# Performance work log

Measured on AMD Instinct MI355X. Metric: run time of the kernel, lower is better.

## Reference

```python
import jax, jax.numpy as jnp
import numpy as np

N, E, F_IN, HID, HEADS, B, CLASSES = 50000, 800000, 128, 64, 4, 512, 2


def setup_inputs() -> dict:
    key = jax.random.key(0)
    ks = jax.random.split(key, 20)
    s = 0.05
    inp = {
        "x": jax.random.normal(ks[0], (N, F_IN), jnp.float32),
        "edge_index": jax.random.randint(ks[1], (2, E), 0, N, jnp.int32),
        "batch": jnp.sort(jax.random.randint(ks[2], (N,), 0, B, jnp.int32)),
        # GCN layers (3): layer0 F_IN->HID, layers 1,2 HID->HID
        "gcn_w0": jax.random.normal(ks[3], (F_IN, HID), jnp.float32) * s,
        "gcn_b0": jnp.zeros((HID,), jnp.float32),
        "gcn_w1": jax.random.normal(ks[4], (HID, HID), jnp.float32) * s,
        "gcn_b1": jnp.zeros((HID,), jnp.float32),
        "gcn_w2": jax.random.normal(ks[5], (HID, HID), jnp.float32) * s,
        "gcn_b2": jnp.zeros((HID,), jnp.float32),
        # GAT: W [HID, HEADS*HID], attention vectors [HEADS, HID], bias [HID] (concat=False)
        "gat_w": jax.random.normal(ks[6], (HID, HEADS * HID), jnp.float32) * s,
        "gat_att_src": jax.random.normal(ks[7], (HEADS, HID), jnp.float32) * s,
        "gat_att_dst": jax.random.normal(ks[8], (HEADS, HID), jnp.float32) * s,
        "gat_b": jnp.zeros((HID,), jnp.float32),
        # MLP head
        "lin1_w": jax.random.normal(ks[9], (HID, HID // 2), jnp.float32) * s,
        "lin1_b": jnp.zeros((HID // 2,), jnp.float32),
        "lin2_w": jax.random.normal(ks[10], (HID // 2, CLASSES), jnp.float32) * s,
        "lin2_b": jnp.zeros((CLASSES,), jnp.float32),
    }
    return inp


def _forward(x, edge_index, batch,
             gcn_w0, gcn_b0, gcn_w1, gcn_b1, gcn_w2, gcn_b2,
             gat_w, gat_att_src, gat_att_dst, gat_b,
             lin1_w, lin1_b, lin2_w, lin2_b):
    n = x.shape[0]
    loop = jnp.arange(n, dtype=edge_index.dtype)
    src = jnp.concatenate([edge_index[0], loop])  # [E+N] with self-loops
    dst = jnp.concatenate([edge_index[1], loop])

    # symmetric GCN normalization (self-loops included, deg >= 1)
    deg = jax.ops.segment_sum(jnp.ones_like(dst, dtype=x.dtype), dst, num_segments=n)
    dinv = jax.lax.rsqrt(jnp.maximum(deg, 1.0))
    norm = dinv[src] * dinv[dst]  # [E+N]

    for W, b in ((gcn_w0, gcn_b0), (gcn_w1, gcn_b1), (gcn_w2, gcn_b2)):
        h = x @ W  # [N, HID]
        x = jax.ops.segment_sum(h[src] * norm[:, None], dst, num_segments=n) + b
        x = jax.nn.relu(x)  # dropout is identity in eval mode

    # GAT layer (heads=HEADS, concat=False -> mean over heads)
    H, C = gat_att_src.shape
    h = (x @ gat_w).reshape(n, H, C)  # [N, H, C]
    a_src = jnp.einsum('nhc,hc->nh', h, gat_att_src)
    a_dst = jnp.einsum('nhc,hc->nh', h, gat_att_dst)
    e = jax.nn.leaky_relu(a_src[src] + a_dst[dst], 0.2)  # [E+N, H]
    m = jax.ops.segment_max(e, dst, num_segments=n)      # per-dst softmax max
    p = jnp.exp(e - m[dst])
    denom = jax.ops.segment_sum(p, dst, num_segments=n)
    alpha = p / denom[dst]                                # [E+N, H]
    out = jax.ops.segment_sum(h[src] * alpha[:, :, None], dst, num_segments=n)
    x = jax.nn.relu(out.mean(axis=1) + gat_b)             # [N, HID]

    # global mean pool + global max pool over graphs
    cnt = jax.ops.segment_sum(jnp.ones((n,), x.dtype), batch, num_segments=B)
    mean_p = jax.ops.segment_sum(x, batch, num_segments=B) / jnp.maximum(cnt, 1.0)[:, None]
    max_p = jax.ops.segment_max(x, batch, num_segments=B)
    max_p = jnp.where(cnt[:, None] > 0, max_p, 0.0)
    g = mean_p + max_p  # [B, HID]

    g = jax.nn.relu(g @ lin1_w + lin1_b)
    return g @ lin2_w + lin2_b  # [B, CLASSES]


def reference(x, edge_index, batch,
              gcn_w0, gcn_b0, gcn_w1, gcn_b1, gcn_w2, gcn_b2,
              gat_w, gat_att_src, gat_att_dst, gat_b,
              lin1_w, lin1_b, lin2_w, lin2_b):
    return _forward(x, edge_index, batch,
                    gcn_w0, gcn_b0, gcn_w1, gcn_b1, gcn_w2, gcn_b2,
                    gat_w, gat_att_src, gat_att_dst, gat_b,
                    lin1_w, lin1_b, lin2_w, lin2_b)
```

## Files before the change

kernel.cpp:

```cpp
#include <hip/hip_runtime.h>
#include <math.h>

typedef short bf8 __attribute__((ext_vector_type(8)));
typedef _Float16 h8 __attribute__((ext_vector_type(8)));
typedef float f4 __attribute__((ext_vector_type(4)));
typedef unsigned short ushort_t;

#define BRANGE 128
#define NB_E 256

__device__ __forceinline__ int ilanebcast(int v, int l) {
  return __builtin_amdgcn_readlane(v, l);
}

__device__ __forceinline__ float wave_sum(float v) {
#pragma unroll
  for (int off = 32; off > 0; off >>= 1) v += __shfl_xor(v, off, 64);
  return v;
}

__device__ __forceinline__ ushort_t f2bf(float x) {
  unsigned int u = __float_as_uint(x);
  return (ushort_t)((u + 0x7fffu + ((u >> 16) & 1u)) >> 16);
}
__device__ __forceinline__ float b2f(ushort_t h) {
  return __uint_as_float(((unsigned int)h) << 16);
}

__global__ __launch_bounds__(256) void k_ehist(const int* __restrict__ dst,
                                               int* __restrict__ bhistT, int E, int nbuk) {
  __shared__ int h[512];
  int b = blockIdx.x, tid = threadIdx.x;
  for (int i = tid; i < nbuk; i += 256) h[i] = 0;
  __syncthreads();
  int chunk = (E + gridDim.x - 1) / gridDim.x;
  int e0 = b * chunk, e1 = min(E, e0 + chunk);
  for (int e = e0 + tid; e < e1; e += 256) atomicAdd(&h[dst[e] >> 7], 1);
  __syncthreads();
  for (int i = tid; i < nbuk; i += 256) bhistT[i * NB_E + b] = h[i];
}

__global__ __launch_bounds__(256) void k_btot(const int* __restrict__ bhistT,
                                              int* __restrict__ bcnt, int nb) {
  __shared__ int sm[256];
  int b = blockIdx.x, tid = threadIdx.x;
  sm[tid] = (tid < nb) ? bhistT[b * NB_E + tid] : 0;
  __syncthreads();
  for (int off = 128; off > 0; off >>= 1) {
    if (tid < off) sm[tid] += sm[tid + off];
    __syncthreads();
  }
  if (tid == 0) bcnt[b] = sm[0];
}

__global__ __launch_bounds__(512) void k_bscan(
    const int* __restrict__ bcnt, int* __restrict__ edgebase, int nbuk,
    int* __restrict__ rowstart, int n, int E) {
  __shared__ int smem[512];
  int t = threadIdx.x;
  int v = (t < nbuk) ? bcnt[t] : 0;
  smem[t] = v;
  __syncthreads();
  for (int off = 1; off < 512; off <<= 1) {
    int u = (t >= off) ? smem[t - off] : 0;
    __syncthreads();
    smem[t] += u;
    __syncthreads();
  }
  if (t < nbuk) edgebase[t] = smem[t] - v;
  if (t == 0) rowstart[n] = E + n;
}

__global__ __launch_bounds__(256) void k_bbase(int* __restrict__ bhistT,
                                               const int* __restrict__ edgebase,
                                               int nb) {
  __shared__ int sm[256];
  int b = blockIdx.x, tid = threadIdx.x;
  int v = (tid < nb) ? bhistT[b * NB_E + tid] : 0;
  sm[tid] = v;
  __syncthreads();
  for (int off = 1; off < 256; off <<= 1) {
    int u = (tid >= off) ? sm[tid - off] : 0;
    __syncthreads();
    sm[tid] += u;
    __syncthreads();
  }
  if (tid < nb) bhistT[b * NB_E + tid] = edgebase[b] + sm[tid] - v;
}

__global__ __launch_bounds__(256) void k_ebucket(
    const int* __restrict__ es, const int* __restrict__ ed,
    const int* __restrict__ bhistT, int* __restrict__ bedges, int E, int nbuk) {
  __shared__ int cur[512];
  int b = blockIdx.x, tid = threadIdx.x;
  for (int i = tid; i < nbuk; i += 256) cur[i] = bhistT[i * NB_E + b];
  __syncthreads();
  int chunk = (E + gridDim.x - 1) / gridDim.x;
  int e0 = b * chunk, e1 = min(E, e0 + chunk);
  for (int e = e0 + tid; e < e1; e += 256) {
    int s = es[e], d = ed[e];
    int pos = atomicAdd(&cur[d >> 7], 1);
    bedges[pos] = (s << 7) | (d & 127);
  }
}

__global__ __launch_bounds__(256) void k_ebsort(
    const int* __restrict__ bedges, const int* __restrict__ edgebase,
    const int* __restrict__ bcnt, int* __restrict__ colidx,
    int* __restrict__ rowstart, float* __restrict__ dinv, int n) {
  __shared__ int h[128];
  __shared__ int c[128];
  int b = blockIdx.x, tid = threadIdx.x;
  int nodes0 = b * BRANGE;
  int nnode = min(BRANGE, n - nodes0);
  int ebase = edgebase[b], ecnt = bcnt[b];
  int colbase = ebase + nodes0;
  if (tid < 128) h[tid] = (tid < nnode) ? 1 : 0;
  __syncthreads();
  for (int k = ebase + tid; k < ebase + ecnt; k += 256)
    atomicAdd(&h[bedges[k] & 127], 1);
  __syncthreads();
  int own = (tid < 128) ? h[tid] : 0;
  for (int off = 1; off < 128; off <<= 1) {
    int t = (tid >= off && tid < 128) ? h[tid - off] : 0;
    __syncthreads();
    if (tid < 128) h[tid] += t;
    __syncthreads();
  }
  if (tid < nnode) {
    int excl = h[tid] - own;
    int node = nodes0 + tid;
    rowstart[node] = colbase + excl;
    dinv[node] = 1.0f / sqrtf((float)own);
    colidx[colbase + excl] = node;
    c[tid] = excl + 1;
  }
  __syncthreads();
  for (int k = ebase + tid; k < ebase + ecnt; k += 256) {
    int p = bedges[k];
    int pos = atomicAdd(&c[p & 127], 1);
    colidx[colbase + pos] = p >> 7;
  }
}


__global__ void k_wswz0(const float* __restrict__ W, ushort_t* __restrict__ Bh,
                        ushort_t* __restrict__ Bl) {
  int e = blockIdx.x * 256 + threadIdx.x;
  if (e >= 4 * 4 * 64) return;
  int lane = e & 63, kc = (e >> 6) & 3, ct = e >> 8;
  int k0 = kc * 32 + (lane >> 4) * 8;
  int col = ct * 16 + (lane & 15);
#pragma unroll
  for (int j = 0; j < 8; j++) {
    float w = W[(k0 + j) * 64 + col];
    ushort_t h = f2bf(w);
    Bh[(size_t)e * 8 + j] = h;
    Bl[(size_t)e * 8 + j] = f2bf(w - b2f(h));
  }
}

__global__ void k_wswz1(const float* __restrict__ W, _Float16* __restrict__ Bh,
                        _Float16* __restrict__ Bl) {
  int e = blockIdx.x * 256 + threadIdx.x;
  if (e >= 8 * 64) return;
  int lane = e & 63, kc = (e >> 6) & 1, ct = e >> 7;
  int k0 = kc * 32 + (lane >> 4) * 8;
  int col = ct * 16 + (lane & 15);
#pragma unroll
  for (int j = 0; j < 8; j++) {
    float w = W[(k0 + j) * 64 + col];
    _Float16 h = (_Float16)w;
    Bh[(size_t)e * 8 + j] = h;
    Bl[(size_t)e * 8 + j] = (_Float16)(w - (float)h);
  }
}

__global__ void k_wswzg(const float* __restrict__ W, ushort_t* __restrict__ Bh,
                        ushort_t* __restrict__ Bl) {
  int e = blockIdx.x * 256 + threadIdx.x;
  if (e >= 4 * 8 * 64) return;
  int lane = e & 63, kc = (e >> 6) & 7, ct = e >> 9;
  int k0 = kc * 32 + (lane >> 4) * 8;
  int col = ct * 16 + (lane & 15);
#pragma unroll
  for (int j = 0; j < 8; j++) {
    int k = k0 + j;
    float w = W[(k & 63) * 256 + (k >> 6) * 64 + col];
    ushort_t h = f2bf(w);
    Bh[(size_t)e * 8 + j] = h;
    Bl[(size_t)e * 8 + j] = f2bf(w - b2f(h));
  }
}

__global__ void k_qpre(const float* __restrict__ W, const float* __restrict__ att_s,
                       const float* __restrict__ att_d,
                       float* __restrict__ q_src, float* __restrict__ q_dst) {
  int t = threadIdx.x;
  int h = t >> 6, k = t & 63;
  float ss = 0.0f, sd = 0.0f;
  for (int c = 0; c < 64; c++) {
    float w = W[k * 256 + h * 64 + c];
    ss = fmaf(w, att_s[h * 64 + c], ss);
    sd = fmaf(w, att_d[h * 64 + c], sd);
  }
  q_src[h * 64 + k] = ss;
  q_dst[h * 64 + k] = sd;
}

__global__ void k_qswz(const float* __restrict__ q_src, const float* __restrict__ q_dst,
                       _Float16* __restrict__ Bq) {
  int e = threadIdx.x;
  if (e >= 128) return;
  int lane = e & 63, kc = e >> 6;
  int k0 = kc * 32 + (lane >> 4) * 8;
  int col = lane & 15;
#pragma unroll
  for (int j = 0; j < 8; j++) {
    int k = k0 + j;
    float v = (col < 4) ? q_src[col * 64 + k]
                        : ((col < 8) ? q_dst[(col - 4) * 64 + k] : 0.0f);
    Bq[(size_t)e * 8 + j] = (_Float16)v;
  }
}

__global__ __launch_bounds__(256) void k_gemm0_mfma(
    const float* __restrict__ X, const ushort_t* __restrict__ Bh,
    const ushort_t* __restrict__ Bl, const float* __restrict__ dinv,
    _Float16* __restrict__ H, int n, int ntiles) {
  int tid = threadIdx.x, lane = tid & 63, wave = tid >> 6;
  int m = lane & 15, q = lane >> 4;
  for (int tile = blockIdx.x * 4 + wave; tile < ntiles; tile += gridDim.x * 4) {
    int ra = tile * 16 + m;
    if (ra >= n) ra = n - 1;
    const float* xrow = X + (size_t)ra * 128;
    f4 acc[4];
#pragma unroll
    for (int ct = 0; ct < 4; ct++) acc[ct] = (f4){0.f, 0.f, 0.f, 0.f};
#pragma unroll 2
    for (int kc = 0; kc < 4; kc++) {
      int ko = kc * 32 + q * 8;
      float4 xa = *(const float4*)(xrow + ko);
      float4 xb = *(const float4*)(xrow + ko + 4);
      float f[8] = {xa.x, xa.y, xa.z, xa.w, xb.x, xb.y, xb.z, xb.w};
      union { ushort_t u[8]; bf8 v; } Uh, Ul;
#pragma unroll
      for (int j = 0; j < 8; j++) {
        ushort_t h = f2bf(f[j]);
        Uh.u[j] = h;
        Ul.u[j] = f2bf(f[j] - b2f(h));
      }
#pragma unroll
      for (int ct = 0; ct < 4; ct++) {
        size_t boff = ((size_t)(ct * 4 + kc) * 64 + lane) * 8;
        bf8 bh = *(const bf8*)(Bh + boff);
        bf8 bl = *(const bf8*)(Bl + boff);
        acc[ct] = __builtin_amdgcn_mfma_f32_16x16x32_bf16(Uh.v, bh, acc[ct], 0, 0, 0);
        acc[ct] = __builtin_amdgcn_mfma_f32_16x16x32_bf16(Ul.v, bh, acc[ct], 0, 0, 0);
        acc[ct] = __builtin_amdgcn_mfma_f32_16x16x32_bf16(Uh.v, bl, acc[ct], 0, 0, 0);
      }
    }
#pragma unroll
    for (int r = 0; r < 4; r++) {
      int row = tile * 16 + q * 4 + r;
      if (row < n) {
        float dv = dinv[row];
#pragma unroll
        for (int ct = 0; ct < 4; ct++)
          H[(size_t)row * 64 + ct * 16 + m] = (_Float16)(acc[ct][r] * dv);
      }
    }
  }
}

__device__ __forceinline__ float gather_sum(const _Float16* __restrict__ h_in,
                                            const int* __restrict__ colidx,
                                            int s0, int s1, int lane) {
  float acc = 0.0f, accB = 0.0f;
  for (int base = s0; base < s1; base += 64) {
    int cnt = min(64, s1 - base);
    int myidx = (lane < cnt) ? colidx[base + lane] : 0;
    int k = 0;
    for (; k + 3 < cnt; k += 4) {
      int sa = ilanebcast(myidx, k);
      int sb = ilanebcast(myidx, k + 1);
      int sc = ilanebcast(myidx, k + 2);
      int sd = ilanebcast(myidx, k + 3);
      float va = (float)h_in[((size_t)sa << 6) + lane];
      float vb = (float)h_in[((size_t)sb << 6) + lane];
      float vc = (float)h_in[((size_t)sc << 6) + lane];
      float vd = (float)h_in[((size_t)sd << 6) + lane];
      acc += va; accB += vb; acc += vc; accB += vd;
    }
    for (; k < cnt; k++) {
      int sa = ilanebcast(myidx, k);
      acc += (float)h_in[((size_t)sa << 6) + lane];
    }
  }
  return acc + accB;
}

__global__ __launch_bounds__(1024) void k_agg_gemm_mfma(
    const _Float16* __restrict__ h_in, const float* __restrict__ dinv,
    const int* __restrict__ rowstart, const int* __restrict__ colidx,
    const float* __restrict__ bias, const _Float16* __restrict__ Bh,
    const _Float16* __restrict__ Bl, _Float16* __restrict__ h_out, int n) {
  __shared__ __align__(16) _Float16 xstage[16][72];
  int tid = threadIdx.x, lane = tid & 63, w = tid >> 6;
  int tile = blockIdx.x;
  int node = tile * 16 + w;
  float xv = 0.0f;
  if (node < n) {
    int s0 = rowstart[node], s1 = rowstart[node + 1];
    float a = gather_sum(h_in, colidx, s0, s1, lane);
    xv = fmaxf(fmaf(dinv[node], a, bias[lane]), 0.0f);
  }
  xstage[w][lane] = (_Float16)xv;
  __syncthreads();
  if (w < 4) {
    int m = lane & 15, q = lane >> 4, ct = w;
    h8 af0 = *(const h8*)&xstage[m][q * 8];
    h8 af1 = *(const h8*)&xstage[m][32 + q * 8];
    size_t o0 = ((size_t)(ct * 2 + 0) * 64 + lane) * 8;
    size_t o1 = ((size_t)(ct * 2 + 1) * 64 + lane) * 8;
    h8 bh0 = *(const h8*)(Bh + o0);
    h8 bh1 = *(const h8*)(Bh + o1);
    h8 bl0 = *(const h8*)(Bl + o0);
    h8 bl1 = *(const h8*)(Bl + o1);
    f4 acc = (f4){0.f, 0.f, 0.f, 0.f};
    acc = __builtin_amdgcn_mfma_f32_16x16x32_f16(af0, bh0, acc, 0, 0, 0);
    acc = __builtin_amdgcn_mfma_f32_16x16x32_f16(af1, bh1, acc, 0, 0, 0);
    acc = __builtin_amdgcn_mfma_f32_16x16x32_f16(af0, bl0, acc, 0, 0, 0);
    acc = __builtin_amdgcn_mfma_f32_16x16x32_f16(af1, bl1, acc, 0, 0, 0);
#pragma unroll
    for (int r = 0; r < 4; r++) {
      int n2 = tile * 16 + q * 4 + r;
      if (n2 < n)
        h_out[(size_t)n2 * 64 + ct * 16 + m] = (_Float16)(acc[r] * dinv[n2]);
    }
  }
}

__global__ __launch_bounds__(1024) void k_agg_gatpre_mfma(
    const _Float16* __restrict__ h_in, const float* __restrict__ dinv,
    const int* __restrict__ rowstart, const int* __restrict__ colidx,
    const float* __restrict__ bias, const _Float16* __restrict__ Bq,
    _Float16* __restrict__ x3, float* __restrict__ a_src, float* __restrict__ a_dst,
    int n) {
  __shared__ __align__(16) _Float16 xstage[16][72];
  int tid = threadIdx.x, lane = tid & 63, w = tid >> 6;
  int tile = blockIdx.x;
  int node = tile * 16 + w;
  float xv = 0.0f;
  if (node < n) {
    int s0 = rowstart[node], s1 = rowstart[node + 1];
    float a = gather_sum(h_in, colidx, s0, s1, lane);
    xv = fmaxf(fmaf(dinv[node], a, bias[lane]), 0.0f);
    x3[((size_t)node << 6) + lane] = (_Float16)xv;
  }
  xstage[w][lane] = (_Float16)xv;
  __syncthreads();
  if (w == 0) {
    int m = lane & 15, q = lane >> 4;
    h8 af0 = *(const h8*)&xstage[m][q * 8];
    h8 af1 = *(const h8*)&xstage[m][32 + q * 8];
    h8 bq0 = *(const h8*)(Bq + (size_t)lane * 8);
    h8 bq1 = *(const h8*)(Bq + (size_t)(64 + lane) * 8);
    f4 accL = (f4){0.f, 0.f, 0.f, 0.f};
    accL = __builtin_amdgcn_mfma_f32_16x16x32_f16(af0, bq0, accL, 0, 0, 0);
    accL = __builtin_amdgcn_mfma_f32_16x16x32_f16(af1, bq1, accL, 0, 0, 0);
#pragma unroll
    for (int r = 0; r < 4; r++) {
      int n2 = tile * 16 + q * 4 + r;
      if (n2 < n) {
        if (m < 4) a_src[(size_t)n2 * 4 + m] = accL[r];
        else if (m < 8) a_dst[(size_t)n2 * 4 + (m - 4)] = accL[r];
      }
    }
  }
}

__global__ __launch_bounds__(256) void k_gat_gather(
    const _Float16* __restrict__ x3, const float* __restrict__ a_src,
    const float* __restrict__ a_dst, const int* __restrict__ rowstart,
    const int* __restrict__ colidx, ushort_t* __restrict__ Ahi,
    ushort_t* __restrict__ Alo, int n) {
  __shared__ __align__(16) float4 wlds[4][64];
  int tid = threadIdx.x, lane = tid & 63, w = tid >> 6;
  int node = blockIdx.x * 4 + w;
  if (node >= n) return;
  const float4 adv = *(const float4*)&a_dst[(size_t)node * 4];
  int s0 = rowstart[node], s1 = rowstart[node + 1];
  float acc0 = 0, acc1 = 0, acc2 = 0, acc3 = 0;
  float S0 = 0, S1 = 0, S2 = 0, S3 = 0;
  for (int base = s0; base < s1; base += 64) {
    int cnt = min(64, s1 - base);
    bool act = (lane < cnt);
    int myidx = act ? colidx[base + lane] : 0;
    float w0 = 0, w1 = 0, w2 = 0, w3 = 0;
    if (act) {
      const float4 as = *(const float4*)&a_src[(size_t)myidx * 4];
      float e0 = as.x + adv.x; e0 = (e0 > 0.f) ? e0 : 0.2f * e0; w0 = __expf(e0);
      float e1 = as.y + adv.y; e1 = (e1 > 0.f) ? e1 : 0.2f * e1; w1 = __expf(e1);
      float e2 = as.z + adv.z; e2 = (e2 > 0.f) ? e2 : 0.2f * e2; w2 = __expf(e2);
      float e3 = as.w + adv.w; e3 = (e3 > 0.f) ? e3 : 0.2f * e3; w3 = __expf(e3);
    }
    S0 += wave_sum(w0); S1 += wave_sum(w1);
    S2 += wave_sum(w2); S3 += wave_sum(w3);
    wlds[w][lane] = make_float4(w0, w1, w2, w3);
    int k = 0;
    for (; k + 3 < cnt; k += 4) {
      int sa = ilanebcast(myidx, k);
      int sb = ilanebcast(myidx, k + 1);
      int sc = ilanebcast(myidx, k + 2);
      int sd = ilanebcast(myidx, k + 3);
      float4 wa = wlds[w][k];
      float4 wb = wlds[w][k + 1];
      float4 wc = wlds[w][k + 2];
      float4 wd = wlds[w][k + 3];
      float va = (float)x3[((size_t)sa << 6) + lane];
      float vb = (float)x3[((size_t)sb << 6) + lane];
      float vc = (float)x3[((size_t)sc << 6) + lane];
      float vd = (float)x3[((size_t)sd << 6) + lane];
      acc0 = fmaf(wa.x, va, acc0); acc1 = fmaf(wa.y, va, acc1);
      acc2 = fmaf(wa.z, va, acc2); acc3 = fmaf(wa.w, va, acc3);
      acc0 = fmaf(wb.x, vb, acc0); acc1 = fmaf(wb.y, vb, acc1);
      acc2 = fmaf(wb.z, vb, acc2); acc3 = fmaf(wb.w, vb, acc3);
      acc0 = fmaf(wc.x, vc, acc0); acc1 = fmaf(wc.y, vc, acc1);
      acc2 = fmaf(wc.z, vc, acc2); acc3 = fmaf(wc.w, vc, acc3);
      acc0 = fmaf(wd.x, vd, acc0); acc1 = fmaf(wd.y, vd, acc1);
      acc2 = fmaf(wd.z, vd, acc2); acc3 = fmaf(wd.w, vd, acc3);
    }
    for (; k < cnt; k++) {
      int sa = ilanebcast(myidx, k);
      float4 wa = wlds[w][k];
      float va = (float)x3[((size_t)sa << 6) + lane];
      acc0 = fmaf(wa.x, va, acc0); acc1 = fmaf(wa.y, va, acc1);
      acc2 = fmaf(wa.z, va, acc2); acc3 = fmaf(wa.w, va, acc3);
    }
  }
  float v[4] = {acc0 * (0.25f / S0), acc1 * (0.25f / S1),
                acc2 * (0.25f / S2), acc3 * (0.25f / S3)};
  size_t baseo = (size_t)node * 256 + lane;
#pragma unroll
  for (int h = 0; h < 4; h++) {
    ushort_t hb = f2bf(v[h]);
    Ahi[baseo + h * 64] = hb;
    Alo[baseo + h * 64] = f2bf(v[h] - b2f(hb));
  }
}

__global__ __launch_bounds__(256) void k_gat_proj_mfma(
    const ushort_t* __restrict__ Ahi, const ushort_t* __restrict__ Alo,
    const ushort_t* __restrict__ Bh, const ushort_t* __restrict__ Bl,
    const float* __restrict__ bias, float* __restrict__ out, int n, int ntiles) {
  int tid = threadIdx.x, lane = tid & 63, wave = tid >> 6;
  int m = lane & 15, q = lane >> 4;
  float bv[4];
#pragma unroll
  for (int ct = 0; ct < 4; ct++) bv[ct] = bias[ct * 16 + m];
  for (int tile = blockIdx.x * 4 + wave; tile < ntiles; tile += gridDim.x * 4) {
    int ra = tile * 16 + m;
    if (ra >= n) ra = n - 1;
    const ushort_t* ahr = Ahi + (size_t)ra * 256;
    const ushort_t* alr = Alo + (size_t)ra * 256;
    f4 acc[4];
#pragma unroll
    for (int ct = 0; ct < 4; ct++) acc[ct] = (f4){0.f, 0.f, 0.f, 0.f};
#pragma unroll 2
    for (int kc = 0; kc < 8; kc++) {
      int ko = kc * 32 + q * 8;
      bf8 ah = *(const bf8*)(ahr + ko);
      bf8 al = *(const bf8*)(alr + ko);
#pragma unroll
      for (int ct = 0; ct < 4; ct++) {
        size_t boff = ((size_t)(ct * 8 + kc) * 64 + lane) * 8;
        bf8 bh = *(const bf8*)(Bh + boff);
        bf8 bl = *(const bf8*)(Bl + boff);
        acc[ct] = __builtin_amdgcn_mfma_f32_16x16x32_bf16(ah, bh, acc[ct], 0, 0, 0);
        acc[ct] = __builtin_amdgcn_mfma_f32_16x16x32_bf16(al, bh, acc[ct], 0, 0, 0);
        acc[ct] = __builtin_amdgcn_mfma_f32_16x16x32_bf16(ah, bl, acc[ct], 0, 0, 0);
      }
    }
#pragma unroll
    for (int r = 0; r < 4; r++) {
      int row = tile * 16 + q * 4 + r;
      if (row < n) {
#pragma unroll
        for (int ct = 0; ct < 4; ct++)
          out[(size_t)row * 64 + ct * 16 + m] = fmaxf(acc[ct][r] + bv[ct], 0.f);
      }
    }
  }
}

__global__ void k_gstart(const int* __restrict__ batch, int* gs, int n, int B) {
  int g = blockIdx.x * blockDim.x + threadIdx.x;
  if (g > B) return;
  int lo = 0, hi = n;
  while (lo < hi) {
    int mid = (lo + hi) >> 1;
    if (batch[mid] < g) lo = mid + 1; else hi = mid;
  }
  gs[g] = lo;
}

__global__ __launch_bounds__(256) void k_pool(const float* __restrict__ x,
                                              const int* __restrict__ gs,
                                              float* __restrict__ gvec, int B) {
  int g = (blockIdx.x * blockDim.x + threadIdx.x) >> 6;
  int lane = threadIdx.x & 63;
  if (g >= B) return;
  int s0 = gs[g], s1 = gs[g + 1];
  float sum = 0.0f, mx = -INFINITY;
  for (int nd = s0; nd < s1; ++nd) {
    float v = x[(size_t)nd * 64 + lane];
    sum += v;
    mx = fmaxf(mx, v);
  }
  int cnt = s1 - s0;
  float mean = sum / fmaxf((float)cnt, 1.0f);
  float mp = (cnt > 0) ? mx : 0.0f;
  gvec[g * 64 + lane] = mean + mp;
}

__global__ __launch_bounds__(256) void k_mlp(const float* __restrict__ gvec,
                                             const float* __restrict__ w1,
                                             const float* __restrict__ b1,
                                             const float* __restrict__ w2,
                                             const float* __restrict__ b2,
                                             float* __restrict__ out, int B) {
  int g = blockIdx.x * blockDim.x + threadIdx.x;
  if (g >= B) return;
  float gv[64];
#pragma unroll
  for (int i = 0; i < 64; i++) gv[i] = gvec[g * 64 + i];
  float o0 = b2[0], o1 = b2[1];
  for (int j = 0; j < 32; j++) {
    float a = b1[j];
#pragma unroll
    for (int i = 0; i < 64; i++) a = fmaf(gv[i], w1[i * 32 + j], a);
    a = fmaxf(a, 0.0f);
    o0 = fmaf(a, w2[j * 2 + 0], o0);
    o1 = fmaf(a, w2[j * 2 + 1], o1);
  }
  out[g * 2 + 0] = o0;
  out[g * 2 + 1] = o1;
}

extern "C" void kernel_launch(void* const* d_in, const int* in_sizes, int n_in,
                              void* d_out, int out_size, void* d_ws, size_t ws_size,
                              hipStream_t stream) {
  const float* x     = (const float*)d_in[0];
  const int*   ei    = (const int*)d_in[1];
  const int*   batch = (const int*)d_in[2];
  const float* w0 = (const float*)d_in[3];  const float* b0 = (const float*)d_in[4];
  const float* w1 = (const float*)d_in[5];  const float* b1 = (const float*)d_in[6];
  const float* w2 = (const float*)d_in[7];  const float* b2 = (const float*)d_in[8];
  const float* gat_w = (const float*)d_in[9];
  const float* att_s = (const float*)d_in[10];
  const float* att_d = (const float*)d_in[11];
  const float* gat_b = (const float*)d_in[12];
  const float* l1w = (const float*)d_in[13]; const float* l1b = (const float*)d_in[14];
  const float* l2w = (const float*)d_in[15]; const float* l2b = (const float*)d_in[16];

  const int N = in_sizes[0] / 128;
  const int E = in_sizes[1] / 2;
  const int B = out_size / 2;
  const int NT = (N + 15) / 16;
  const int NBUK = (N + BRANGE - 1) / BRANGE;

  char* ws = (char*)d_ws;
  size_t off = 0;
  auto alloc = [&](size_t bytes) -> void* {
    void* p = ws + off;
    off = (off + bytes + 255) & ~(size_t)255;
    return p;
  };
  int*       bhistT   = (int*)alloc((size_t)NBUK * NB_E * 4);
  int*       edgebase = (int*)alloc((size_t)NBUK * 4);
  int*       bcnt     = (int*)alloc((size_t)NBUK * 4);
  int*       bedges   = (int*)alloc((size_t)E * 4);
  int*       rowstart = (int*)alloc((size_t)(N + 1) * 4);
  int*       colidx   = (int*)alloc((size_t)(E + N) * 4);
  float*     dinv     = (float*)alloc((size_t)N * 4);
  _Float16*  hbuf     = (_Float16*)alloc((size_t)N * 64 * 2);
  _Float16*  hbuf2    = (_Float16*)alloc((size_t)N * 64 * 2);
  _Float16*  xg       = (_Float16*)alloc((size_t)N * 64 * 2);
  float*     gatout   = (float*)alloc((size_t)N * 64 * 4);
  ushort_t*  Ahi      = (ushort_t*)alloc((size_t)N * 256 * 2);
  ushort_t*  Alo      = (ushort_t*)alloc((size_t)N * 256 * 2);
  float*     a_src    = (float*)alloc((size_t)N * 4 * 4);
  float*     a_dst    = (float*)alloc((size_t)N * 4 * 4);
  float*     q_src    = (float*)alloc(4 * 64 * 4);
  float*     q_dst    = (float*)alloc(4 * 64 * 4);
  ushort_t*  B0h      = (ushort_t*)alloc(4 * 4 * 64 * 8 * 2);
  ushort_t*  B0l      = (ushort_t*)alloc(4 * 4 * 64 * 8 * 2);
  _Float16*  Bw1h     = (_Float16*)alloc(8 * 64 * 8 * 2);
  _Float16*  Bw1l     = (_Float16*)alloc(8 * 64 * 8 * 2);
  _Float16*  Bw2h     = (_Float16*)alloc(8 * 64 * 8 * 2);
  _Float16*  Bw2l     = (_Float16*)alloc(8 * 64 * 8 * 2);
  _Float16*  Bq       = (_Float16*)alloc(2 * 64 * 8 * 2);
  ushort_t*  Bgh      = (ushort_t*)alloc(4 * 8 * 64 * 8 * 2);
  ushort_t*  Bgl      = (ushort_t*)alloc(4 * 8 * 64 * 8 * 2);
  int*       gs       = (int*)alloc((size_t)(B + 1) * 4);
  float*     gvec     = (float*)alloc((size_t)B * 64 * 4);
  (void)ws_size; (void)n_in;

  k_ehist<<<NB_E, 256, 0, stream>>>(ei + E, bhistT, E, NBUK);
  k_btot<<<NBUK, 256, 0, stream>>>(bhistT, bcnt, NB_E);
  k_bscan<<<1, 512, 0, stream>>>(bcnt, edgebase, NBUK, rowstart, N, E);
  k_bbase<<<NBUK, 256, 0, stream>>>(bhistT, edgebase, NB_E);
  k_ebucket<<<NB_E, 256, 0, stream>>>(ei, ei + E, bhistT, bedges, E, NBUK);
  k_ebsort<<<NBUK, 256, 0, stream>>>(bedges, edgebase, bcnt, colidx, rowstart, dinv, N);
  k_qpre<<<1, 256, 0, stream>>>(gat_w, att_s, att_d, q_src, q_dst);
  k_qswz<<<1, 256, 0, stream>>>(q_src, q_dst, Bq);
  k_wswz0<<<4, 256, 0, stream>>>(w0, B0h, B0l);
  k_wswz1<<<2, 256, 0, stream>>>(w1, Bw1h, Bw1l);
  k_wswz1<<<2, 256, 0, stream>>>(w2, Bw2h, Bw2l);
  k_wswzg<<<8, 256, 0, stream>>>(gat_w, Bgh, Bgl);

  k_gemm0_mfma<<<1024, 256, 0, stream>>>(x, B0h, B0l, dinv, hbuf, N, NT);
  k_agg_gemm_mfma<<<NT, 1024, 0, stream>>>(hbuf, dinv, rowstart, colidx, b0,
                                           Bw1h, Bw1l, hbuf2, N);
  k_agg_gemm_mfma<<<NT, 1024, 0, stream>>>(hbuf2, dinv, rowstart, colidx, b1,
                                           Bw2h, Bw2l, hbuf, N);
  k_agg_gatpre_mfma<<<NT, 1024, 0, stream>>>(hbuf, dinv, rowstart, colidx, b2,
                                             Bq, xg, a_src, a_dst, N);
  k_gat_gather<<<(N + 3) / 4, 256, 0, stream>>>(xg, a_src, a_dst, rowstart, colidx,
                                                Ahi, Alo, N);
  k_gat_proj_mfma<<<1024, 256, 0, stream>>>(Ahi, Alo, Bgh, Bgl, gat_b, gatout, N, NT);
  k_gstart<<<(B + 1 + 255) / 256, 256, 0, stream>>>(batch, gs, N, B);
  k_pool<<<(B + 3) / 4, 256, 0, stream>>>(gatout, gs, gvec, B);
  k_mlp<<<(B + 255) / 256, 256, 0, stream>>>(gvec, l1w, l1b, l2w, l2b, (float*)d_out, B);
}
```

Baseline: 376.9 us.

## Fuse GAT attention gather with output projection MFMA via shared-memory staging

Merges the GAT gather kernel and the GAT projection GEMM into one 1024-thread block per 16-node tile. Each block keeps the per-head aggregated features in LDS instead of writing bf16 hi/lo split buffers (N*256*2*2 bytes) to global memory and reading them back. The projection weights switch from a bf16 hi/lo split to an fp16 hi/lo split, and the activations are split in-register before the MFMA. The trade-offs are that only 4 of the 16 waves run the projection, a block-wide barrier follows the irregular gather, and the larger blocks may lower occupancy.

```diff
diff --git a/kernel.cpp b/kernel.cpp
--- a/kernel.cpp
+++ b/kernel.cpp
@@ -176,8 +176,8 @@
   }
 }
 
-__global__ void k_wswzg(const float* __restrict__ W, ushort_t* __restrict__ Bh,
-                        ushort_t* __restrict__ Bl) {
+__global__ void k_wswzg(const float* __restrict__ W, _Float16* __restrict__ Bh,
+                        _Float16* __restrict__ Bl) {
   int e = blockIdx.x * 256 + threadIdx.x;
   if (e >= 4 * 8 * 64) return;
   int lane = e & 63, kc = (e >> 6) & 7, ct = e >> 9;
@@ -187,9 +187,9 @@
   for (int j = 0; j < 8; j++) {
     int k = k0 + j;
     float w = W[(k & 63) * 256 + (k >> 6) * 64 + col];
-    ushort_t h = f2bf(w);
+    _Float16 h = (_Float16)w;
     Bh[(size_t)e * 8 + j] = h;
-    Bl[(size_t)e * 8 + j] = f2bf(w - b2f(h));
+    Bl[(size_t)e * 8 + j] = (_Float16)(w - (float)h);
   }
 }
 
@@ -380,116 +380,106 @@
   }
 }
 
-__global__ __launch_bounds__(256) void k_gat_gather(
+__global__ __launch_bounds__(1024) void k_gat_fused(
     const _Float16* __restrict__ x3, const float* __restrict__ a_src,
     const float* __restrict__ a_dst, const int* __restrict__ rowstart,
-    const int* __restrict__ colidx, ushort_t* __restrict__ Ahi,
-    ushort_t* __restrict__ Alo, int n) {
-  __shared__ __align__(16) float4 wlds[4][64];
+    const int* __restrict__ colidx, const _Float16* __restrict__ Bh,
+    const _Float16* __restrict__ Bl, const float* __restrict__ bias,
+    float* __restrict__ out, int n) {
+  __shared__ __align__(16) float4 wlds[16][64];
+  __shared__ __align__(16) float astage[16][260];
   int tid = threadIdx.x, lane = tid & 63, w = tid >> 6;
-  int node = blockIdx.x * 4 + w;
-  if (node >= n) return;
-  const float4 adv = *(const float4*)&a_dst[(size_t)node * 4];
-  int s0 = rowstart[node], s1 = rowstart[node + 1];
-  float acc0 = 0, acc1 = 0, acc2 = 0, acc3 = 0;
-  float S0 = 0, S1 = 0, S2 = 0, S3 = 0;
-  for (int base = s0; base < s1; base += 64) {
-    int cnt = min(64, s1 - base);
-    bool act = (lane < cnt);
-    int myidx = act ? colidx[base + lane] : 0;
-    float w0 = 0, w1 = 0, w2 = 0, w3 = 0;
-    if (act) {
-      const float4 as = *(const float4*)&a_src[(size_t)myidx * 4];
-      float e0 = as.x + adv.x; e0 = (e0 > 0.f) ? e0 : 0.2f * e0; w0 = __expf(e0);
-      float e1 = as.y + adv.y; e1 = (e1 > 0.f) ? e1 : 0.2f * e1; w1 = __expf(e1);
-      float e2 = as.z + adv.z; e2 = (e2 > 0.f) ? e2 : 0.2f * e2; w2 = __expf(e2);
-      float e3 = as.w + adv.w; e3 = (e3 > 0.f) ? e3 : 0.2f * e3; w3 = __expf(e3);
-    }
-    S0 += wave_sum(w0); S1 += wave_sum(w1);
-    S2 += wave_sum(w2); S3 += wave_sum(w3);
-    wlds[w][lane] = make_float4(w0, w1, w2, w3);
-    int k = 0;
-    for (; k + 3 < cnt; k += 4) {
-      int sa = ilanebcast(myidx, k);
-      int sb = ilanebcast(myidx, k + 1);
-      int sc = ilanebcast(myidx, k + 2);
-      int sd = ilanebcast(myidx, k + 3);
-      float4 wa = wlds[w][k];
-      float4 wb = wlds[w][k + 1];
-      float4 wc = wlds[w][k + 2];
-      float4 wd = wlds[w][k + 3];
-      float va = (float)x3[((size_t)sa << 6) + lane];
-      float vb = (float)x3[((size_t)sb << 6) + lane];
-      float vc = (float)x3[((size_t)sc << 6) + lane];
-      float vd = (float)x3[((size_t)sd << 6) + lane];
-      acc0 = fmaf(wa.x, va, acc0); acc1 = fmaf(wa.y, va, acc1);
-      acc2 = fmaf(wa.z, va, acc2); acc3 = fmaf(wa.w, va, acc3);
-      acc0 = fmaf(wb.x, vb, acc0); acc1 = fmaf(wb.y, vb, acc1);
-      acc2 = fmaf(wb.z, vb, acc2); acc3 = fmaf(wb.w, vb, acc3);
-      acc0 = fmaf(wc.x, vc, acc0); acc1 = fmaf(wc.y, vc, acc1);
-      acc2 = fmaf(wc.z, vc, acc2); acc3 = fmaf(wc.w, vc, acc3);
-      acc0 = fmaf(wd.x, vd, acc0); acc1 = fmaf(wd.y, vd, acc1);
-      acc2 = fmaf(wd.z, vd, acc2); acc3 = fmaf(wd.w, vd, acc3);
-    }
-    for (; k < cnt; k++) {
-      int sa = ilanebcast(myidx, k);
-      float4 wa = wlds[w][k];
-      float va = (float)x3[((size_t)sa << 6) + lane];
-      acc0 = fmaf(wa.x, va, acc0); acc1 = fmaf(wa.y, va, acc1);
-      acc2 = fmaf(wa.z, va, acc2); acc3 = fmaf(wa.w, va, acc3);
-    }
-  }
-  float v[4] = {acc0 * (0.25f / S0), acc1 * (0.25f / S1),
-                acc2 * (0.25f / S2), acc3 * (0.25f / S3)};
-  size_t baseo = (size_t)node * 256 + lane;
-#pragma unroll
-  for (int h = 0; h < 4; h++) {
-    ushort_t hb = f2bf(v[h]);
-    Ahi[baseo + h * 64] = hb;
-    Alo[baseo + h * 64] = f2bf(v[h] - b2f(hb));
-  }
-}
-
-__global__ __launch_bounds__(256) void k_gat_proj_mfma(
-    const ushort_t* __restrict__ Ahi, const ushort_t* __restrict__ Alo,
-    const ushort_t* __restrict__ Bh, const ushort_t* __restrict__ Bl,
-    const float* __restrict__ bias, float* __restrict__ out, int n, int ntiles) {
-  int tid = threadIdx.x, lane = tid & 63, wave = tid >> 6;
-  int m = lane & 15, q = lane >> 4;
-  float bv[4];
-#pragma unroll
-  for (int ct = 0; ct < 4; ct++) bv[ct] = bias[ct * 16 + m];
-  for (int tile = blockIdx.x * 4 + wave; tile < ntiles; tile += gridDim.x * 4) {
-    int ra = tile * 16 + m;
-    if (ra >= n) ra = n - 1;
-    const ushort_t* ahr = Ahi + (size_t)ra * 256;
-    const ushort_t* alr = Alo + (size_t)ra * 256;
-    f4 acc[4];
-#pragma unroll
-    for (int ct = 0; ct < 4; ct++) acc[ct] = (f4){0.f, 0.f, 0.f, 0.f};
+  int tile = blockIdx.x;
+  int node = tile * 16 + w;
+  float v0 = 0.f, v1 = 0.f, v2 = 0.f, v3 = 0.f;
+  if (node < n) {
+    const float4 adv = *(const float4*)&a_dst[(size_t)node * 4];
+    int s0 = rowstart[node], s1 = rowstart[node + 1];
+    float acc0 = 0, acc1 = 0, acc2 = 0, acc3 = 0;
+    float S0 = 0, S1 = 0, S2 = 0, S3 = 0;
+    for (int base = s0; base < s1; base += 64) {
+      int cnt = min(64, s1 - base);
+      bool act = (lane < cnt);
+      int myidx = act ? colidx[base + lane] : 0;
+      float w0 = 0, w1 = 0, w2 = 0, w3 = 0;
+      if (act) {
+        const float4 as = *(const float4*)&a_src[(size_t)myidx * 4];
+        float e0 = as.x + adv.x; e0 = (e0 > 0.f) ? e0 : 0.2f * e0; w0 = __expf(e0);
+        float e1 = as.y + adv.y; e1 = (e1 > 0.f) ? e1 : 0.2f * e1; w1 = __expf(e1);
+        float e2 = as.z + adv.z; e2 = (e2 > 0.f) ? e2 : 0.2f * e2; w2 = __expf(e2);
+        float e3 = as.w + adv.w; e3 = (e3 > 0.f) ? e3 : 0.2f * e3; w3 = __expf(e3);
+      }
+      S0 += wave_sum(w0); S1 += wave_sum(w1);
+      S2 += wave_sum(w2); S3 += wave_sum(w3);
+      wlds[w][lane] = make_float4(w0, w1, w2, w3);
+      int k = 0;
+      for (; k + 3 < cnt; k += 4) {
+        int sa = ilanebcast(myidx, k);
+        int sb = ilanebcast(myidx, k + 1);
+        int sc = ilanebcast(myidx, k + 2);
+        int sd = ilanebcast(myidx, k + 3);
+        float4 wa = wlds[w][k];
+        float4 wb = wlds[w][k + 1];
+        float4 wc = wlds[w][k + 2];
+        float4 wd = wlds[w][k + 3];
+        float va = (float)x3[((size_t)sa << 6) + lane];
+        float vb = (float)x3[((size_t)sb << 6) + lane];
+        float vc = (float)x3[((size_t)sc << 6) + lane];
+        float vd = (float)x3[((size_t)sd << 6) + lane];
+        acc0 = fmaf(wa.x, va, acc0); acc1 = fmaf(wa.y, va, acc1);
+        acc2 = fmaf(wa.z, va, acc2); acc3 = fmaf(wa.w, va, acc3);
+        acc0 = fmaf(wb.x, vb, acc0); acc1 = fmaf(wb.y, vb, acc1);
+        acc2 = fmaf(wb.z, vb, acc2); acc3 = fmaf(wb.w, vb, acc3);
+        acc0 = fmaf(wc.x, vc, acc0); acc1 = fmaf(wc.y, vc, acc1);
+        acc2 = fmaf(wc.z, vc, acc2); acc3 = fmaf(wc.w, vc, acc3);
+        acc0 = fmaf(wd.x, vd, acc0); acc1 = fmaf(wd.y, vd, acc1);
+        acc2 = fmaf(wd.z, vd, acc2); acc3 = fmaf(wd.w, vd, acc3);
+      }
+      for (; k < cnt; k++) {
+        int sa = ilanebcast(myidx, k);
+        float4 wa = wlds[w][k];
+        float va = (float)x3[((size_t)sa << 6) + lane];
+        acc0 = fmaf(wa.x, va, acc0); acc1 = fmaf(wa.y, va, acc1);
+        acc2 = fmaf(wa.z, va, acc2); acc3 = fmaf(wa.w, va, acc3);
+      }
+    }
+    v0 = acc0 * (0.25f / S0);
+    v1 = acc1 * (0.25f / S1);
+    v2 = acc2 * (0.25f / S2);
+    v3 = acc3 * (0.25f / S3);
+  }
+  astage[w][lane] = v0;
+  astage[w][64 + lane] = v1;
+  astage[w][128 + lane] = v2;
+  astage[w][192 + lane] = v3;
+  __syncthreads();
+  if (w < 4) {
+    int m = lane & 15, q = lane >> 4, ct = w;
+    float bv = bias[ct * 16 + m];
+    f4 acc = (f4){0.f, 0.f, 0.f, 0.f};
 #pragma unroll 2
     for (int kc = 0; kc < 8; kc++) {
-      int ko = kc * 32 + q * 8;
-      bf8 ah = *(const bf8*)(ahr + ko);
-      bf8 al = *(const bf8*)(alr + ko);
-#pragma unroll
-      for (int ct = 0; ct < 4; ct++) {
-        size_t boff = ((size_t)(ct * 8 + kc) * 64 + lane) * 8;
-        bf8 bh = *(const bf8*)(Bh + boff);
-        bf8 bl = *(const bf8*)(Bl + boff);
-        acc[ct] = __builtin_amdgcn_mfma_f32_16x16x32_bf16(ah, bh, acc[ct], 0, 0, 0);
-        acc[ct] = __builtin_amdgcn_mfma_f32_16x16x32_bf16(al, bh, acc[ct], 0, 0, 0);
-        acc[ct] = __builtin_amdgcn_mfma_f32_16x16x32_bf16(ah, bl, acc[ct], 0, 0, 0);
-      }
+      const float* ap = &astage[m][kc * 32 + q * 8];
+      union { _Float16 u[8]; h8 v; } Uh, Ul;
+#pragma unroll
+      for (int j = 0; j < 8; j++) {
+        float a = ap[j];
+        _Float16 h = (_Float16)a;
+        Uh.u[j] = h;
+        Ul.u[j] = (_Float16)(a - (float)h);
+      }
+      size_t boff = ((size_t)(ct * 8 + kc) * 64 + lane) * 8;
+      h8 bh = *(const h8*)(Bh + boff);
+      h8 bl = *(const h8*)(Bl + boff);
+      acc = __builtin_amdgcn_mfma_f32_16x16x32_f16(Uh.v, bh, acc, 0, 0, 0);
+      acc = __builtin_amdgcn_mfma_f32_16x16x32_f16(Ul.v, bh, acc, 0, 0, 0);
+      acc = __builtin_amdgcn_mfma_f32_16x16x32_f16(Uh.v, bl, acc, 0, 0, 0);
     }
 #pragma unroll
     for (int r = 0; r < 4; r++) {
       int row = tile * 16 + q * 4 + r;
-      if (row < n) {
-#pragma unroll
-        for (int ct = 0; ct < 4; ct++)
-          out[(size_t)row * 64 + ct * 16 + m] = fmaxf(acc[ct][r] + bv[ct], 0.f);
-      }
+      if (row < n)
+        out[(size_t)row * 64 + ct * 16 + m] = fmaxf(acc[r] + bv, 0.f);
     }
   }
 }
@@ -588,8 +578,6 @@
   _Float16*  hbuf2    = (_Float16*)alloc((size_t)N * 64 * 2);
   _Float16*  xg       = (_Float16*)alloc((size_t)N * 64 * 2);
   float*     gatout   = (float*)alloc((size_t)N * 64 * 4);
-  ushort_t*  Ahi      = (ushort_t*)alloc((size_t)N * 256 * 2);
-  ushort_t*  Alo      = (ushort_t*)alloc((size_t)N * 256 * 2);
   float*     a_src    = (float*)alloc((size_t)N * 4 * 4);
   float*     a_dst    = (float*)alloc((size_t)N * 4 * 4);
   float*     q_src    = (float*)alloc(4 * 64 * 4);
@@ -601,8 +589,8 @@
   _Float16*  Bw2h     = (_Float16*)alloc(8 * 64 * 8 * 2);
   _Float16*  Bw2l     = (_Float16*)alloc(8 * 64 * 8 * 2);
   _Float16*  Bq       = (_Float16*)alloc(2 * 64 * 8 * 2);
-  ushort_t*  Bgh      = (ushort_t*)alloc(4 * 8 * 64 * 8 * 2);
-  ushort_t*  Bgl      = (ushort_t*)alloc(4 * 8 * 64 * 8 * 2);
+  _Float16*  Bgh      = (_Float16*)alloc(4 * 8 * 64 * 8 * 2);
+  _Float16*  Bgl      = (_Float16*)alloc(4 * 8 * 64 * 8 * 2);
   int*       gs       = (int*)alloc((size_t)(B + 1) * 4);
   float*     gvec     = (float*)alloc((size_t)B * 64 * 4);
   (void)ws_size; (void)n_in;
@@ -627,9 +615,8 @@
                                            Bw2h, Bw2l, hbuf, N);
   k_agg_gatpre_mfma<<<NT, 1024, 0, stream>>>(hbuf, dinv, rowstart, colidx, b2,
                                              Bq, xg, a_src, a_dst, N);
-  k_gat_gather<<<(N + 3) / 4, 256, 0, stream>>>(xg, a_src, a_dst, rowstart, colidx,
-                                                Ahi, Alo, N);
-  k_gat_proj_mfma<<<1024, 256, 0, stream>>>(Ahi, Alo, Bgh, Bgl, gat_b, gatout, N, NT);
+  k_gat_fused<<<NT, 1024, 0, stream>>>(xg, a_src, a_dst, rowstart, colidx,
+                                       Bgh, Bgl, gat_b, gatout, N);
   k_gstart<<<(B + 1 + 255) / 256, 256, 0, stream>>>(batch, gs, N, B);
   k_pool<<<(B + 3) / 4, 256, 0, stream>>>(gatout, gs, gvec, B);
   k_mlp<<<(B + 255) / 256, 256, 0, stream>>>(gvec, l1w, l1b, l2w, l2b, (float*)d_out, B);
```

Measured after the change: 373.4 us. About the same (-0.9%).
